# Optimization experiments

Hardware: AMD Instinct MI355X
Metric: run time of the kernel (lower is better)

Reference implementation:

```python
import jax, jax.numpy as jnp
import numpy as np

# 'linear' blur taps from the source module
_KERNEL_1D = np.array([1/8, 3/8, 3/8, 1/8], dtype=np.float32)


def setup_inputs() -> dict:
    key = jax.random.key(0)
    B, C, H, W = 8, 256, 256, 256
    x = jax.random.normal(key, (B, C, H, W), dtype=jnp.float32)
    # 2D separable blur kernel: outer product of the 1D taps (registered buffer)
    kernel = jnp.asarray(np.outer(_KERNEL_1D, _KERNEL_1D))  # [4, 4]
    return {"x": x, "kernel": kernel}


def reference(x, kernel):
    # pad = k//2 - 1 = 1, reflect padding (torch 'reflect' == numpy 'reflect')
    pad = kernel.shape[0] // 2 - 1
    xp = jnp.pad(x, ((0, 0), (0, 0), (pad, pad), (pad, pad)), mode="reflect")
    C = x.shape[1]
    # Original builds a C x C weight that is zero off-diagonal; math is exactly a
    # depthwise (per-channel) conv with the same 4x4 blur kernel, stride 2.
    w = jnp.broadcast_to(kernel, (C, 1) + kernel.shape)  # [C, 1, 4, 4]
    out = jax.lax.conv_general_dilated(
        xp, w,
        window_strides=(2, 2),
        padding="VALID",
        dimension_numbers=("NCHW", "OIHW", "NCHW"),
        feature_group_count=C,
    )
    return out
```

## Files before the change

kernel.cpp:

```cpp
#include <hip/hip_runtime.h>


#define K0 0.125f
#define K1 0.375f

__global__ __launch_bounds__(256, 4) void downsample2d_kernel(
    const float* __restrict__ x, float* __restrict__ out)
{
    __shared__ float lds[34 * 256];

    const int tid   = threadIdx.x;
    const int strip = blockIdx.x & 7;
    const int plane = blockIdx.x >> 3;
    const int oh0   = strip * 16;
    const int ir0   = 2 * oh0 - 1;

    const float* xp = x + (size_t)plane * (256 * 256);

    const int lin0 = tid << 2;
    #pragma unroll
    for (int i = 0; i < 9; ++i) {
        int linear = i * 1024 + lin0;
        int r = linear >> 8;
        if (r < 34) {
            int c  = linear & 255;
            int gr = ir0 + r;
            gr = (gr < 0) ? 1 : ((gr > 255) ? 254 : gr);
            float4 v = *(const float4*)(xp + gr * 256 + c);
            *(float4*)(&lds[linear]) = v;
        }
    }
    __syncthreads();

    const int ow   = tid & 127;
    const int half = tid >> 7;
    const float* L = lds + (half << 4) * 256;

    const int c1 = 2 * ow;
    const float* pm = L + ((ow == 0)   ? 1   : c1 - 1);
    const float* p0 = L + c1;
    const float* pp = L + ((ow == 127) ? 254 : c1 + 2);

    auto H = [&](int lr) {
        int o = lr * 256;
        return K0 * pm[o] + K1 * p0[o] + K1 * p0[o + 1] + K0 * pp[o];
    };

    float* op = out + (size_t)plane * (128 * 128)
                    + (size_t)(oh0 + (half << 3)) * 128 + ow;

    float h0 = H(0);
    float h1 = H(1);
    #pragma unroll
    for (int l = 0; l < 8; ++l) {
        float h2 = H(2 * l + 2);
        float h3 = H(2 * l + 3);
        op[l * 128] = K0 * h0 + K1 * h1 + K1 * h2 + K0 * h3;
        h0 = h2;
        h1 = h3;
    }
}

extern "C" void kernel_launch(void* const* d_in, const int* in_sizes, int n_in,
                              void* d_out, int out_size, void* d_ws, size_t ws_size,
                              hipStream_t stream) {
    const float* x = (const float*)d_in[0];
    float* out = (float*)d_out;

    const int planes = 8 * 256;
    const int blocks = planes * 8;
    downsample2d_kernel<<<blocks, 256, 0, stream>>>(x, out);
}
```

Before: 706.7 us.

## Do horizontal blur pass in registers with wave shuffles before LDS

The horizontal 4-tap filter now runs right after each global row load, using wavefront shuffles to get neighbouring columns, so only the half-width horizontally filtered rows go to LDS. This halves the LDS footprint and removes the redundant horizontal recomputation and strided LDS reads in the vertical pass. The launch bound is raised to 8 blocks per CU to use the smaller LDS footprint. The trade-off is shuffle instructions and more register pressure, and the kernel is likely still bound by memory bandwidth.

Result: no change. 712.4 us (+0.8%).

```diff
diff --git a/kernel.cpp b/kernel.cpp
--- a/kernel.cpp
+++ b/kernel.cpp
@@ -4,10 +4,10 @@
 #define K0 0.125f
 #define K1 0.375f
 
-__global__ __launch_bounds__(256, 4) void downsample2d_kernel(
+__global__ __launch_bounds__(256, 8) void downsample2d_kernel(
     const float* __restrict__ x, float* __restrict__ out)
 {
-    __shared__ float lds[34 * 256];
+    __shared__ float ldsH[34 * 128];
 
     const int tid   = threadIdx.x;
     const int strip = blockIdx.x & 7;
@@ -17,44 +17,40 @@
 
     const float* xp = x + (size_t)plane * (256 * 256);
 
-    const int lin0 = tid << 2;
+    const int lane = tid & 63;
+    const int wave = tid >> 6;
+
     #pragma unroll
     for (int i = 0; i < 9; ++i) {
-        int linear = i * 1024 + lin0;
-        int r = linear >> 8;
+        int r = wave + 4 * i;
         if (r < 34) {
-            int c  = linear & 255;
             int gr = ir0 + r;
             gr = (gr < 0) ? 1 : ((gr > 255) ? 254 : gr);
-            float4 v = *(const float4*)(xp + gr * 256 + c);
-            *(float4*)(&lds[linear]) = v;
+            float4 v = *(const float4*)(xp + gr * 256 + (lane << 2));
+            float xm1 = __shfl_up(v.w, 1);
+            float xp4 = __shfl_down(v.x, 1);
+            if (lane == 0)  xm1 = v.y;
+            if (lane == 63) xp4 = v.z;
+            float h0 = K0 * xm1 + K1 * v.x + K1 * v.y + K0 * v.z;
+            float h1 = K0 * v.y + K1 * v.z + K1 * v.w + K0 * xp4;
+            *(float2*)(&ldsH[r * 128 + (lane << 1)]) = make_float2(h0, h1);
         }
     }
     __syncthreads();
 
     const int ow   = tid & 127;
     const int half = tid >> 7;
-    const float* L = lds + (half << 4) * 256;
-
-    const int c1 = 2 * ow;
-    const float* pm = L + ((ow == 0)   ? 1   : c1 - 1);
-    const float* p0 = L + c1;
-    const float* pp = L + ((ow == 127) ? 254 : c1 + 2);
-
-    auto H = [&](int lr) {
-        int o = lr * 256;
-        return K0 * pm[o] + K1 * p0[o] + K1 * p0[o + 1] + K0 * pp[o];
-    };
+    const float* L = ldsH + (half << 4) * 128 + ow;
 
     float* op = out + (size_t)plane * (128 * 128)
                     + (size_t)(oh0 + (half << 3)) * 128 + ow;
 
-    float h0 = H(0);
-    float h1 = H(1);
+    float h0 = L[0];
+    float h1 = L[128];
     #pragma unroll
     for (int l = 0; l < 8; ++l) {
-        float h2 = H(2 * l + 2);
-        float h3 = H(2 * l + 3);
+        float h2 = L[(2 * l + 2) * 128];
+        float h3 = L[(2 * l + 3) * 128];
         op[l * 128] = K0 * h0 + K1 * h1 + K1 * h2 + K0 * h3;
         h0 = h2;
         h1 = h3;
```
